# Performance work log

Measured on AMD Instinct MI355X. Metric: run time of the kernel, lower is better.

## Reference

```python
import jax, jax.numpy as jnp
import numpy as np

NUM_HEADS = 12
TOP_K = 2
ROPE_THETA = 10000.0
EPS = 1e-6

def _rmsnorm(x, w):
    return x * jax.lax.rsqrt(jnp.mean(x * x, axis=-1, keepdims=True) + EPS) * w

def _rotate_half(t):
    t1, t2 = jnp.split(t, 2, axis=-1)
    return jnp.concatenate([-t2, t1], axis=-1)

def setup_inputs() -> dict:
    key = jax.random.key(0)
    ks = jax.random.split(key, 8)
    B, S, H, E, F = 2, 2048, 768, 8, 3072
    s = 0.02
    return {
        "x": jax.random.normal(ks[0], (B, S, H), dtype=jnp.float32),
        "attn_norm_w": jnp.ones((H,), dtype=jnp.float32),
        "wqkv": jax.random.normal(ks[1], (H, 3 * H), dtype=jnp.float32) * s,
        "wo": jax.random.normal(ks[2], (H, H), dtype=jnp.float32) * s,
        "ffn_norm_w": jnp.ones((H,), dtype=jnp.float32),
        "router_w": jax.random.normal(ks[3], (H, E), dtype=jnp.float32) * s,
        "w1": jax.random.normal(ks[4], (E, H, F), dtype=jnp.float32) * s,
        "w2": jax.random.normal(ks[5], (E, F, H), dtype=jnp.float32) * s,
    }

def reference(x, attn_norm_w, wqkv, wo, ffn_norm_w, router_w, w1, w2):
    B, S, H = x.shape
    NH, Dh = NUM_HEADS, H // NUM_HEADS
    E = router_w.shape[1]

    # ---- attention sub-block: x = x + attn(rmsnorm(x)) ----
    h = _rmsnorm(x, attn_norm_w)
    qkv = h @ wqkv  # (B,S,3H)
    q, k, v = [t.reshape(B, S, NH, Dh) for t in jnp.split(qkv, 3, axis=-1)]

    # RoPE (llama-style half-split rotation)
    half = Dh // 2
    inv_freq = 1.0 / (ROPE_THETA ** (jnp.arange(half, dtype=jnp.float32) / half))
    ang = jnp.arange(S, dtype=jnp.float32)[:, None] * inv_freq[None, :]  # (S, half)
    cos = jnp.concatenate([jnp.cos(ang)] * 2, axis=-1)[None, :, None, :].astype(x.dtype)
    sin = jnp.concatenate([jnp.sin(ang)] * 2, axis=-1)[None, :, None, :].astype(x.dtype)
    q = q * cos + _rotate_half(q) * sin
    k = k * cos + _rotate_half(k) * sin

    scores = jnp.einsum('bqhd,bkhd->bhqk', q, k) / jnp.sqrt(jnp.asarray(Dh, x.dtype))
    causal = jnp.tril(jnp.ones((S, S), dtype=bool))
    scores = jnp.where(causal[None, None], scores, jnp.asarray(-1e9, x.dtype))
    attn = jax.nn.softmax(scores, axis=-1)
    o = jnp.einsum('bhqk,bkhd->bqhd', attn, v).reshape(B, S, H) @ wo
    x = x + o

    # ---- MoE FFN sub-block: x = x + moe(rmsnorm(x)) ----
    hn = _rmsnorm(x, ffn_norm_w).reshape(-1, H)  # (T,H)
    logits = hn @ router_w  # (T,E)
    probs = jax.nn.softmax(logits, axis=-1)
    top_v, top_i = jax.lax.top_k(probs, TOP_K)  # (T,K)
    top_v = top_v / jnp.sum(top_v, axis=-1, keepdims=True)
    onehot = jax.nn.one_hot(top_i, E, dtype=x.dtype)  # (T,K,E)
    combine = jnp.einsum('tke,tk->te', onehot, top_v)  # (T,E)

    h1 = jnp.einsum('th,ehf->etf', hn, w1)
    h2 = jnp.einsum('etf,efh->eth', jax.nn.silu(h1), w2)
    moe_out = jnp.einsum('eth,te->th', h2, combine).reshape(B, S, H)

    # load-balancing aux loss (switch-style)
    frac = jnp.mean(jnp.sum(onehot, axis=1), axis=0) / TOP_K  # (E,)
    mean_prob = jnp.mean(probs, axis=0)  # (E,)
    aux = jnp.asarray(E, x.dtype) * jnp.sum(frac * mean_prob)

    return (x + moe_out, aux)
```

## Files before the change

kernel.cpp:

```cpp
#include <hip/hip_runtime.h>
#include <cstdint>
#include <cstddef>

typedef __bf16 bf16;
typedef bf16 bf16x8 __attribute__((ext_vector_type(8)));
typedef float f32x4 __attribute__((ext_vector_type(4)));

__device__ __forceinline__ void async_cp16(const void* g, void* l) {
    __builtin_amdgcn_global_load_lds(
        (const __attribute__((address_space(1))) unsigned int*)(unsigned long long)g,
        (__attribute__((address_space(3))) unsigned int*)(unsigned int)(unsigned long long)l,
        16, 0, 0);
}

#define BARX() __builtin_amdgcn_s_barrier()
#define LGKM0() asm volatile("s_waitcnt lgkmcnt(0)" ::: "memory")
#define VMC4() asm volatile("s_waitcnt vmcnt(4)" ::: "memory")
#define VMC0() asm volatile("s_waitcnt vmcnt(0)" ::: "memory")

__global__ __launch_bounds__(256) void transpose_cast(const float* __restrict__ in,
                                                      bf16* __restrict__ out, int R, int C) {
    __shared__ float tile[32][33];
    int bz = blockIdx.z;
    in  += (size_t)bz * R * C;
    out += (size_t)bz * R * C;
    int c0 = blockIdx.x * 32, r0 = blockIdx.y * 32;
    int tx = threadIdx.x & 31, ty = threadIdx.x >> 5;
#pragma unroll
    for (int i = 0; i < 4; ++i)
        tile[ty + i * 8][tx] = in[(size_t)(r0 + ty + i * 8) * C + c0 + tx];
    __syncthreads();
#pragma unroll
    for (int i = 0; i < 4; ++i)
        out[(size_t)(c0 + ty + i * 8) * R + r0 + tx] = (bf16)tile[tx][ty + i * 8];
}

__global__ __launch_bounds__(256) void rmsnorm_cast(const float* __restrict__ x,
                                                    const float* __restrict__ w,
                                                    bf16* __restrict__ out) {
    int row = blockIdx.x, tid = threadIdx.x;
    const float* xr = x + (size_t)row * 768;
    float v0 = xr[tid], v1 = xr[tid + 256], v2 = xr[tid + 512];
    float s = v0 * v0 + v1 * v1 + v2 * v2;
#pragma unroll
    for (int off = 32; off; off >>= 1) s += __shfl_xor(s, off, 64);
    __shared__ float red[4];
    if ((tid & 63) == 0) red[tid >> 6] = s;
    __syncthreads();
    float tot = red[0] + red[1] + red[2] + red[3];
    float rs = rsqrtf(tot * (1.f / 768.f) + 1e-6f);
    bf16* o = out + (size_t)row * 768;
    o[tid]       = (bf16)(v0 * rs * w[tid]);
    o[tid + 256] = (bf16)(v1 * rs * w[tid + 256]);
    o[tid + 512] = (bf16)(v2 * rs * w[tid + 512]);
}

__global__ __launch_bounds__(256) void rope_kernel(const bf16* __restrict__ qkv,
                                                   bf16* __restrict__ qb,
                                                   bf16* __restrict__ kb,
                                                   bf16* __restrict__ vtb) {
    __shared__ float vs[64][65];
    const int tid = threadIdx.x;
    const int s0 = blockIdx.x * 64, bh = blockIdx.y;
    const int b = bh / 12, h = bh - b * 12;
    const float qscale = 0.18033688f;
#pragma unroll
    for (int i = 0; i < 16; ++i) {
        int idx = i * 256 + tid;
        int sl = idx >> 6, d = idx & 63;
        int sg = s0 + sl;
        size_t base = ((size_t)b * 2048 + sg) * 2304;
        float qv = (float)qkv[base + h * 64 + d];
        float kv = (float)qkv[base + 768 + h * 64 + d];
        float vv = (float)qkv[base + 1536 + h * 64 + d];
        float qp = (float)qkv[base + h * 64 + (d ^ 32)];
        float kp = (float)qkv[base + 768 + h * 64 + (d ^ 32)];
        int jj = d & 31;
        float invf = __expf(-(float)jj * (9.210340371976184f / 32.f));
        float ang = (float)sg * invf;
        float cv, sv;
        __sincosf(ang, &sv, &cv);
        float rq = (d < 32) ? -qp : qp;
        float rk = (d < 32) ? -kp : kp;
        qb[((size_t)bh * 2048 + sg) * 64 + d] = (bf16)((qv * cv + rq * sv) * qscale);
        kb[((size_t)bh * 2048 + sg) * 64 + d] = (bf16)(kv * cv + rk * sv);
        vs[sl][d] = vv;
    }
    __syncthreads();
#pragma unroll
    for (int i = 0; i < 16; ++i) {
        int idx = i * 256 + tid;
        int d = idx >> 6, sl = idx & 63;
        vtb[(size_t)bh * 64 * 2048 + (size_t)d * 2048 + s0 + sl] = (bf16)vs[sl][d];
    }
}

__global__ __launch_bounds__(256) void attn_kernel(const bf16* __restrict__ qb,
                                                   const bf16* __restrict__ kb,
                                                   const bf16* __restrict__ vtb,
                                                   bf16* __restrict__ ob) {
    __shared__ __align__(16) bf16 Qs[2][64][32];
    __shared__ __align__(16) bf16 Ks[2][2][64][32];
    __shared__ __align__(16) bf16 Vts[2][2][64][32];
    __shared__ __align__(16) bf16 Ps[4][1024];

    const int tid = threadIdx.x, lane = tid & 63, w = tid >> 6;
    const int quad = lane >> 4, l16 = lane & 15;
    const int linear = (int)blockIdx.y * 32 + (int)blockIdx.x;
    const int xcd = linear & 7, j = linear >> 3;
    const int bh = xcd * 3 + (j >> 5);
    const int qt = 31 - (j & 31);
    const int q0 = qt * 64;
    const int b = bh / 12, h = bh - b * 12;

    const bf16* qhead = qb + (size_t)bh * 2048 * 64;
    const bf16* khead = kb + (size_t)bh * 2048 * 64;
    const bf16* vthead = vtb + (size_t)bh * 64 * 2048;

#pragma unroll
    for (int i = 0; i < 2; ++i) {
        int o = (i * 256 + tid) * 16;
        int kk = o >> 12, row = (o >> 6) & 63, el = (o & 63) >> 1;
        async_cp16(qhead + (size_t)(q0 + row) * 64 + kk * 32 + el,
                   (char*)Qs + (size_t)(i * 256 + w * 64) * 16);
    }
    __syncthreads();
    bf16x8 bq[2];
#pragma unroll
    for (int kk = 0; kk < 2; ++kk)
        bq[kk] = *(const bf16x8*)&Qs[kk][w * 16 + l16][quad * 8];

    f32x4 o_acc[4] = {};
    float m_st = -1e30f, l_st = 0.f;

    for (int j2 = 0; j2 <= qt; j2 += 2) {
        int nt2 = (j2 + 1 <= qt) ? 2 : 1;
        __syncthreads();
#pragma unroll
        for (int t = 0; t < 2; ++t) {
            if (t >= nt2) break;
            int kv0 = (j2 + t) * 64;
#pragma unroll
            for (int i = 0; i < 2; ++i) {
                int o = (i * 256 + tid) * 16;
                int kk = o >> 12, row = (o >> 6) & 63, el = (o & 63) >> 1;
                async_cp16(khead + (size_t)(kv0 + row) * 64 + kk * 32 + el,
                           (char*)&Ks[t] + (size_t)(i * 256 + w * 64) * 16);
                async_cp16(vthead + (size_t)row * 2048 + kv0 + kk * 32 + el,
                           (char*)&Vts[t] + (size_t)(i * 256 + w * 64) * 16);
            }
        }
        __syncthreads();

#pragma unroll
        for (int t = 0; t < 2; ++t) {
            if (t >= nt2) break;

            f32x4 sacc[4] = {};
#pragma unroll
            for (int kk = 0; kk < 2; ++kk) {
                bf16x8 ak[4];
#pragma unroll
                for (int ni = 0; ni < 4; ++ni)
                    ak[ni] = *(const bf16x8*)&Ks[t][kk][ni * 16 + l16][quad * 8];
#pragma unroll
                for (int ni = 0; ni < 4; ++ni)
                    sacc[ni] = __builtin_amdgcn_mfma_f32_16x16x32_bf16(ak[ni], bq[kk], sacc[ni], 0, 0, 0);
            }

            if (j2 + t == qt) {
                int ql = w * 16 + l16;
#pragma unroll
                for (int ni = 0; ni < 4; ++ni)
#pragma unroll
                    for (int r = 0; r < 4; ++r)
                        if (ni * 16 + quad * 4 + r > ql) sacc[ni][r] = -1e30f;
            }

            float mx = sacc[0][0];
#pragma unroll
            for (int ni = 0; ni < 4; ++ni)
#pragma unroll
                for (int r = 0; r < 4; ++r) mx = fmaxf(mx, sacc[ni][r]);
            mx = fmaxf(mx, __shfl_xor(mx, 16, 64));
            mx = fmaxf(mx, __shfl_xor(mx, 32, 64));
            float mnew = fmaxf(m_st, mx);
            float alpha = exp2f(m_st - mnew);
            m_st = mnew;
            float rsum = 0.f;
#pragma unroll
            for (int ni = 0; ni < 4; ++ni)
#pragma unroll
                for (int r = 0; r < 4; ++r) {
                    float pv = exp2f(sacc[ni][r] - mnew);
                    sacc[ni][r] = pv;
                    rsum += pv;
                }
            rsum += __shfl_xor(rsum, 16, 64);
            rsum += __shfl_xor(rsum, 32, 64);
            l_st = l_st * alpha + rsum;

            float af[4];
#pragma unroll
            for (int r = 0; r < 4; ++r) af[r] = __shfl(alpha, quad * 4 + r, 64);
#pragma unroll
            for (int ni = 0; ni < 4; ++ni)
#pragma unroll
                for (int r = 0; r < 4; ++r) o_acc[ni][r] *= af[r];

            bf16* pb = Ps[w];
#pragma unroll
            for (int ni = 0; ni < 4; ++ni)
#pragma unroll
                for (int r = 0; r < 4; ++r) {
                    int kv = ni * 16 + quad * 4 + r;
                    int ch = (kv >> 3) ^ (l16 & 7);
                    pb[l16 * 64 + ch * 8 + (kv & 7)] = (bf16)sacc[ni][r];
                }

#pragma unroll
            for (int kk = 0; kk < 2; ++kk) {
                int ch = (kk * 4 + quad) ^ (l16 & 7);
                bf16x8 ap = *(const bf16x8*)&pb[l16 * 64 + ch * 8];
                bf16x8 bv[4];
#pragma unroll
                for (int ni = 0; ni < 4; ++ni)
                    bv[ni] = *(const bf16x8*)&Vts[t][kk][ni * 16 + l16][quad * 8];
#pragma unroll
                for (int ni = 0; ni < 4; ++ni)
                    o_acc[ni] = __builtin_amdgcn_mfma_f32_16x16x32_bf16(ap, bv[ni], o_acc[ni], 0, 0, 0);
            }
        }
    }

    float lf[4];
#pragma unroll
    for (int r = 0; r < 4; ++r) lf[r] = 1.f / __shfl(l_st, quad * 4 + r, 64);
#pragma unroll
    for (int ni = 0; ni < 4; ++ni)
#pragma unroll
        for (int r = 0; r < 4; ++r) {
            int rowg = q0 + w * 16 + quad * 4 + r;
            size_t tk = (size_t)b * 2048 + rowg;
            ob[tk * 768 + h * 64 + ni * 16 + l16] = (bf16)(o_acc[ni][r] * lf[r]);
        }
}

__global__ __launch_bounds__(256) void rms_router(const float* __restrict__ x1,
                                                  const float* __restrict__ w,
                                                  const float* __restrict__ rw,
                                                  bf16* __restrict__ hn,
                                                  int* __restrict__ topi,
                                                  float* __restrict__ topw,
                                                  float* __restrict__ probsb) {
    __shared__ float hnf[768];
    __shared__ float part[256];
    __shared__ float lg[8];
    __shared__ float probs[8];
    __shared__ float red[4];
    int row = blockIdx.x, tid = threadIdx.x;
    const float* xr = x1 + (size_t)row * 768;
    float v0 = xr[tid], v1 = xr[tid + 256], v2 = xr[tid + 512];
    float s = v0 * v0 + v1 * v1 + v2 * v2;
#pragma unroll
    for (int off = 32; off; off >>= 1) s += __shfl_xor(s, off, 64);
    if ((tid & 63) == 0) red[tid >> 6] = s;
    __syncthreads();
    float tot = red[0] + red[1] + red[2] + red[3];
    float rs = rsqrtf(tot * (1.f / 768.f) + 1e-6f);
    float h0 = v0 * rs * w[tid], h1v = v1 * rs * w[tid + 256], h2v = v2 * rs * w[tid + 512];
    hnf[tid] = h0; hnf[tid + 256] = h1v; hnf[tid + 512] = h2v;
    bf16* o = hn + (size_t)row * 768;
    o[tid] = (bf16)h0; o[tid + 256] = (bf16)h1v; o[tid + 512] = (bf16)h2v;
    __syncthreads();
    int e = tid & 7, seg = tid >> 3;
    float p = 0.f;
#pragma unroll
    for (int j = 0; j < 24; ++j) { int k = seg * 24 + j; p += hnf[k] * rw[k * 8 + e]; }
    part[tid] = p;
    __syncthreads();
    if (tid < 8) { float a = 0.f; for (int sgi = 0; sgi < 32; ++sgi) a += part[sgi * 8 + tid]; lg[tid] = a; }
    __syncthreads();
    if (tid == 0) {
        float mx = lg[0];
        for (int i = 1; i < 8; ++i) mx = fmaxf(mx, lg[i]);
        float ssum = 0.f, ex[8];
        for (int i = 0; i < 8; ++i) { ex[i] = __expf(lg[i] - mx); ssum += ex[i]; }
        float inv = 1.f / ssum;
        for (int i = 0; i < 8; ++i) probs[i] = ex[i] * inv;
        int e0 = 0; float p0 = probs[0];
        for (int i = 1; i < 8; ++i) if (probs[i] > p0) { p0 = probs[i]; e0 = i; }
        int e1 = -1; float p1 = -1.f;
        for (int i = 0; i < 8; ++i) if (i != e0 && probs[i] > p1) { p1 = probs[i]; e1 = i; }
        float wsum = p0 + p1;
        topi[row * 2] = e0; topi[row * 2 + 1] = e1;
        topw[row * 2] = p0 / wsum; topw[row * 2 + 1] = p1 / wsum;
    }
    __syncthreads();
    if (tid < 8) probsb[(size_t)row * 8 + tid] = probs[tid];
}

__global__ __launch_bounds__(256) void router_stats(const float* __restrict__ probsb,
                                                    const int* __restrict__ topi,
                                                    int* ctrl, int4* tiles, float* auxOut) {
    __shared__ float pws[4][8];
    __shared__ int cws[4][8];
    int tid = threadIdx.x;
    float s[8] = {};
    int cnt[8] = {};
    for (int t = tid; t < 4096; t += 256) {
        const float4* p = (const float4*)(probsb + (size_t)t * 8);
        float4 a = p[0], b = p[1];
        s[0] += a.x; s[1] += a.y; s[2] += a.z; s[3] += a.w;
        s[4] += b.x; s[5] += b.y; s[6] += b.z; s[7] += b.w;
        int e0 = topi[2 * t], e1 = topi[2 * t + 1];
#pragma unroll
        for (int e = 0; e < 8; ++e) cnt[e] += (e == e0) + (e == e1);
    }
#pragma unroll
    for (int e = 0; e < 8; ++e)
#pragma unroll
        for (int off = 32; off; off >>= 1) {
            s[e] += __shfl_xor(s[e], off, 64);
            cnt[e] += __shfl_xor(cnt[e], off, 64);
        }
    if ((tid & 63) == 0) {
#pragma unroll
        for (int e = 0; e < 8; ++e) { pws[tid >> 6][e] = s[e]; cws[tid >> 6][e] = cnt[e]; }
    }
    __syncthreads();
    if (tid == 0) {
        int off = 0, nt = 0;
        float aux = 0.f;
        for (int e = 0; e < 8; ++e) {
            int ne = cws[0][e] + cws[1][e] + cws[2][e] + cws[3][e];
            float ps = pws[0][e] + pws[1][e] + pws[2][e] + pws[3][e];
            ctrl[e] = ne;
            ctrl[32 + e] = off;
            int ntl = (ne + 255) >> 8;
            for (int i = 0; i < ntl; ++i) { tiles[nt] = make_int4(e, off + i * 256, off + ne, 0); ++nt; }
            off += ntl << 8;
            aux += ((float)ne * (1.f / 8192.f)) * (ps * (1.f / 4096.f));
        }
        ctrl[24] = nt;
        auxOut[0] = 8.f * aux;
    }
}

__global__ __launch_bounds__(256) void place_tokens(const int* __restrict__ topi,
                                                    int* ctrl, int* __restrict__ perm,
                                                    int* __restrict__ tokslot) {
    __shared__ int lcnt[8], lbase[8];
    int tid = threadIdx.x;
    int t = blockIdx.x * 256 + tid;
    if (tid < 8) lcnt[tid] = 0;
    __syncthreads();
    int e0 = topi[2 * t], e1 = topi[2 * t + 1];
    int p0 = atomicAdd(&lcnt[e0], 1);
    int p1 = atomicAdd(&lcnt[e1], 1);
    __syncthreads();
    if (tid < 8) lbase[tid] = atomicAdd(&ctrl[16 + tid], lcnt[tid]);
    __syncthreads();
    int g0 = ctrl[32 + e0] + lbase[e0] + p0;
    int g1 = ctrl[32 + e1] + lbase[e1] + p1;
    perm[g0] = t; perm[g1] = t;
    tokslot[2 * t] = g0; tokslot[2 * t + 1] = g1;
}

__global__ __launch_bounds__(256) void moe_combine(const bf16* __restrict__ h2,
                                                   const int* __restrict__ tokslot,
                                                   const float* __restrict__ topw,
                                                   float* __restrict__ out) {
    int t = blockIdx.x, tid = threadIdx.x;
    int s0 = tokslot[2 * t], s1 = tokslot[2 * t + 1];
    float w0 = topw[2 * t], w1 = topw[2 * t + 1];
    const bf16* r0 = h2 + (size_t)s0 * 768;
    const bf16* r1 = h2 + (size_t)s1 * 768;
    float* o = out + (size_t)t * 768;
#pragma unroll
    for (int i = 0; i < 3; ++i) {
        int c = i * 256 + tid;
        o[c] += w0 * (float)r0[c] + w1 * (float)r1[c];
    }
}

template <int MODE>
__global__ __launch_bounds__(512, 2) void gemm8p(const bf16* __restrict__ A,
                                                 const bf16* __restrict__ Bt,
                                                 int N, int K,
                                                 bf16* __restrict__ outB,
                                                 const int4* __restrict__ tiles,
                                                 const int* __restrict__ ctrl,
                                                 const int* __restrict__ perm) {
    __shared__ __align__(16) bf16 As[2][2][128 * 64];
    __shared__ __align__(16) bf16 Bs[2][2][128 * 64];
    __shared__ int sPerm[256];

    const int tid = threadIdx.x, lane = tid & 63, wid = tid >> 6;
    const int wr = wid >> 2, wc = wid & 3;
    const int quad = lane >> 4, l16 = lane & 15;

    const int NB = N >> 8;
    const int mt = (int)blockIdx.x / NB;
    const int n0 = ((int)blockIdx.x % NB) << 8;

    int m0 = 0, row0 = 0;
    if (MODE == 0) {
        m0 = mt << 8;
    } else {
        if (mt >= ctrl[24]) return;
        int4 td = tiles[mt];
        row0 = td.y;
        Bt += (size_t)td.x * (size_t)N * K;
        if (tid < 256) {
            int g = row0 + tid;
            sPerm[tid] = perm[(g < td.z) ? g : row0];
        }
        __syncthreads();
    }

    const int r0t = tid >> 3;
    const int s0t = tid & 7;
    const int cOff = ((s0t ^ (r0t & 7)) << 3);
    const bf16* pA[2][2];
    const bf16* pB[2][2];
#pragma unroll
    for (int h = 0; h < 2; ++h)
#pragma unroll
        for (int i = 0; i < 2; ++i) {
            int rrow = h * 128 + i * 64 + r0t;
            pB[h][i] = Bt + (size_t)(n0 + rrow) * K + cOff;
            if (MODE == 0) pA[h][i] = A + (size_t)(m0 + rrow) * K + cOff;
            else           pA[h][i] = A + (size_t)sPerm[rrow] * K + cOff;
        }

    auto stA = [&](int buf, int h, int kt) {
#pragma unroll
        for (int i = 0; i < 2; ++i)
            async_cp16(pA[h][i] + kt, (char*)As[buf][h] + (size_t)((i * 512 + wid * 64) * 16));
    };
    auto stB = [&](int buf, int h, int kt) {
#pragma unroll
        for (int i = 0; i < 2; ++i)
            async_cp16(pB[h][i] + kt, (char*)Bs[buf][h] + (size_t)((i * 512 + wid * 64) * 16));
    };
    auto ldA = [&](int buf, int mi, int kk) -> bf16x8 {
        int r = mi * 16 + l16;
        int s = (kk * 4 + quad) ^ (l16 & 7);
        return *(const bf16x8*)((const char*)As[buf][wr] + r * 128 + s * 16);
    };
    auto ldB = [&](int buf, int ni, int kk) -> bf16x8 {
        int c = wc * 64 + ni * 16 + l16;
        int s = (kk * 4 + quad) ^ (l16 & 7);
        return *(const bf16x8*)((const char*)Bs[buf][c >> 7] + (c & 127) * 128 + s * 16);
    };

    f32x4 acc[8][4] = {};
    bf16x8 aLo[4][2], aHi[4][2], bLo[2][2], bHi[2][2];

    auto ktile = [&](int b, auto S1, auto S2, auto S3, auto S4, int vm) {
#pragma unroll
        for (int mi = 0; mi < 4; ++mi) { aLo[mi][0] = ldA(b, mi, 0); aLo[mi][1] = ldA(b, mi, 1); }
#pragma unroll
        for (int ni = 0; ni < 2; ++ni) { bLo[ni][0] = ldB(b, ni, 0); bLo[ni][1] = ldB(b, ni, 1); }
        S1();
        BARX(); LGKM0();
        __builtin_amdgcn_s_setprio(1);
#pragma unroll
        for (int mi = 0; mi < 4; ++mi)
#pragma unroll
            for (int ni = 0; ni < 2; ++ni) {
                acc[mi][ni] = __builtin_amdgcn_mfma_f32_16x16x32_bf16(aLo[mi][0], bLo[ni][0], acc[mi][ni], 0, 0, 0);
                acc[mi][ni] = __builtin_amdgcn_mfma_f32_16x16x32_bf16(aLo[mi][1], bLo[ni][1], acc[mi][ni], 0, 0, 0);
            }
        __builtin_amdgcn_s_setprio(0);
        BARX();
#pragma unroll
        for (int ni = 0; ni < 2; ++ni) { bHi[ni][0] = ldB(b, ni + 2, 0); bHi[ni][1] = ldB(b, ni + 2, 1); }
        S2();
        BARX(); LGKM0();
        __builtin_amdgcn_s_setprio(1);
#pragma unroll
        for (int mi = 0; mi < 4; ++mi)
#pragma unroll
            for (int ni = 0; ni < 2; ++ni) {
                acc[mi][ni + 2] = __builtin_amdgcn_mfma_f32_16x16x32_bf16(aLo[mi][0], bHi[ni][0], acc[mi][ni + 2], 0, 0, 0);
                acc[mi][ni + 2] = __builtin_amdgcn_mfma_f32_16x16x32_bf16(aLo[mi][1], bHi[ni][1], acc[mi][ni + 2], 0, 0, 0);
            }
        __builtin_amdgcn_s_setprio(0);
        BARX();
#pragma unroll
        for (int mi = 0; mi < 4; ++mi) { aHi[mi][0] = ldA(b, mi + 4, 0); aHi[mi][1] = ldA(b, mi + 4, 1); }
        S3();
        BARX(); LGKM0();
        __builtin_amdgcn_s_setprio(1);
#pragma unroll
        for (int mi = 0; mi < 4; ++mi)
#pragma unroll
            for (int ni = 0; ni < 2; ++ni) {
                acc[mi + 4][ni + 2] = __builtin_amdgcn_mfma_f32_16x16x32_bf16(aHi[mi][0], bHi[ni][0], acc[mi + 4][ni + 2], 0, 0, 0);
                acc[mi + 4][ni + 2] = __builtin_amdgcn_mfma_f32_16x16x32_bf16(aHi[mi][1], bHi[ni][1], acc[mi + 4][ni + 2], 0, 0, 0);
            }
        __builtin_amdgcn_s_setprio(0);
        BARX();
        S4();
        BARX(); LGKM0();
        __builtin_amdgcn_s_setprio(1);
#pragma unroll
        for (int mi = 0; mi < 4; ++mi)
#pragma unroll
            for (int ni = 0; ni < 2; ++ni) {
                acc[mi + 4][ni] = __builtin_amdgcn_mfma_f32_16x16x32_bf16(aHi[mi][0], bLo[ni][0], acc[mi + 4][ni], 0, 0, 0);
                acc[mi + 4][ni] = __builtin_amdgcn_mfma_f32_16x16x32_bf16(aHi[mi][1], bLo[ni][1], acc[mi + 4][ni], 0, 0, 0);
            }
        __builtin_amdgcn_s_setprio(0);
        if (vm == 4) { VMC4(); } else if (vm == 0) { VMC0(); }
        BARX();
    };

    stA(0, 0, 0); stA(0, 1, 0); stB(0, 0, 0); stB(0, 1, 0);
    stB(1, 0, 64); stB(1, 1, 64);
    VMC4();
    BARX();

    const int nIt = K >> 7;
    for (int it = 0; it < nIt; ++it) {
        const bool last = (it == nIt - 1);
        const int kA = (it * 2 + 1) << 6;
        const int kB = (it * 2 + 2) << 6;
        const int kC = (it * 2 + 3) << 6;
        ktile(0,
              [&] { stA(1, 0, kA); },
              [&] { stA(1, 1, kA); },
              [&] { if (!last) stB(0, 0, kB); },
              [&] { if (!last) stB(0, 1, kB); },
              last ? 0 : 4);
        ktile(1,
              [&] { if (!last) stA(0, 0, kB); },
              [&] { if (!last) stA(0, 1, kB); },
              [&] { if (!last) stB(1, 0, kC); },
              [&] { if (!last) stB(1, 1, kC); },
              last ? -1 : 4);
    }

#pragma unroll
    for (int mi = 0; mi < 8; ++mi)
#pragma unroll
        for (int ni = 0; ni < 4; ++ni)
#pragma unroll
            for (int r = 0; r < 4; ++r) {
                int lrow = wr * 128 + mi * 16 + quad * 4 + r;
                int col  = n0 + wc * 64 + ni * 16 + l16;
                float v = acc[mi][ni][r];
                if (MODE == 0) {
                    outB[(size_t)(m0 + lrow) * N + col] = (bf16)v;
                } else {
                    float sv = v / (1.f + __expf(-v));
                    outB[(size_t)(row0 + lrow) * N + col] = (bf16)sv;
                }
            }
}

template <int MODE, int NBX, int MTX>
__global__ __launch_bounds__(256) void gemm_nt(const bf16* __restrict__ A,
                                               const bf16* __restrict__ Bt,
                                               int N, int K,
                                               const float* __restrict__ xres,
                                               float* __restrict__ outF,
                                               bf16* __restrict__ outB,
                                               const int4* __restrict__ tiles,
                                               const int* __restrict__ ctrl,
                                               const int* __restrict__ perm) {
    __shared__ __align__(16) bf16 As[2][128 * 32];
    __shared__ __align__(16) bf16 Bs[2][128 * 32];
    __shared__ int sPerm[128];

    const int tid = threadIdx.x, lane = tid & 63, w = tid >> 6;
    const int wr = w >> 1, wc = w & 1, quad = lane >> 4, l16 = lane & 15;

    const int L = blockIdx.x;
    const int xcd = L & 7, j = L >> 3;
    const int mt = xcd * MTX + j / NBX;
    const int n0 = (j % NBX) * 128;

    int m0 = 0, row0 = 0;
    if (MODE <= 1) {
        m0 = mt * 128;
    } else if (MODE == 2) {
        if (mt >= ctrl[24]) return;
        int4 td = tiles[mt];
        row0 = td.y;
        int rowend = td.z;
        Bt += (size_t)td.x * N * K;
        if (tid < 128) {
            int g = row0 + tid;
            int gs = (g < rowend) ? g : row0;
            sPerm[tid] = perm[gs];
        }
        __syncthreads();
    } else {
        int tt = mt >> 1;
        if (tt >= ctrl[24]) return;
        int4 td = tiles[tt];
        row0 = td.y + ((mt & 1) << 7);
        Bt += (size_t)td.x * N * K;
    }

    auto stage = [&](int buf, int kt) {
#pragma unroll
        for (int i = 0; i < 2; ++i) {
            int c = i * 256 + tid;
            int r = c >> 2, koff = (c & 3) * 8;
            const bf16* gp;
            if (MODE == 2)      gp = A + (size_t)sPerm[r] * K + kt + koff;
            else if (MODE == 3) gp = A + (size_t)(row0 + r) * K + kt + koff;
            else                gp = A + (size_t)(m0 + r) * K + kt + koff;
            async_cp16(gp, (char*)As[buf] + (size_t)(i * 256 + w * 64) * 16);
            async_cp16(Bt + (size_t)(n0 + r) * K + kt + koff,
                       (char*)Bs[buf] + (size_t)(i * 256 + w * 64) * 16);
        }
    };

    f32x4 acc[4][4] = {};
    const int nIt = K >> 5;
    stage(0, 0);

    for (int it = 0; it < nIt; ++it) {
        const int cur = it & 1;
        __syncthreads();
        if (it + 1 < nIt) stage(cur ^ 1, (it + 1) << 5);

        bf16x8 af[4], bfr[4];
#pragma unroll
        for (int mi = 0; mi < 4; ++mi)
            af[mi] = *(const bf16x8*)(As[cur] + (wr * 64 + mi * 16 + l16) * 32 + quad * 8);
#pragma unroll
        for (int ni = 0; ni < 4; ++ni)
            bfr[ni] = *(const bf16x8*)(Bs[cur] + (wc * 64 + ni * 16 + l16) * 32 + quad * 8);
#pragma unroll
        for (int mi = 0; mi < 4; ++mi)
#pragma unroll
            for (int ni = 0; ni < 4; ++ni)
                acc[mi][ni] = __builtin_amdgcn_mfma_f32_16x16x32_bf16(af[mi], bfr[ni], acc[mi][ni], 0, 0, 0);
    }

#pragma unroll
    for (int mi = 0; mi < 4; ++mi)
#pragma unroll
        for (int ni = 0; ni < 4; ++ni)
#pragma unroll
            for (int r = 0; r < 4; ++r) {
                int lrow = wr * 64 + mi * 16 + quad * 4 + r;
                int col = n0 + wc * 64 + ni * 16 + l16;
                float v = acc[mi][ni][r];
                if (MODE == 0) {
                    outB[(size_t)(m0 + lrow) * N + col] = (bf16)v;
                } else if (MODE == 1) {
                    size_t idx = (size_t)(m0 + lrow) * N + col;
                    outF[idx] = v + xres[idx];
                } else if (MODE == 2) {
                    float sv = v / (1.f + __expf(-v));
                    outB[(size_t)(row0 + lrow) * N + col] = (bf16)sv;
                } else {
                    outB[(size_t)(row0 + lrow) * N + col] = (bf16)v;
                }
            }
}

__global__ void zero_ctrl(int* ctrl) { if (threadIdx.x < 64) ctrl[threadIdx.x] = 0; }

extern "C" void kernel_launch(void* const* d_in, const int* in_sizes, int n_in,
                              void* d_out, int out_size, void* d_ws, size_t ws_size,
                              hipStream_t stream) {
    const float* x    = (const float*)d_in[0];
    const float* anw  = (const float*)d_in[1];
    const float* wqkv = (const float*)d_in[2];
    const float* wo   = (const float*)d_in[3];
    const float* fnw  = (const float*)d_in[4];
    const float* rw   = (const float*)d_in[5];
    const float* w1   = (const float*)d_in[6];
    const float* w2   = (const float*)d_in[7];
    float* out = (float*)d_out;

    char* ws = (char*)d_ws;
    size_t off = 0;
    auto alloc = [&](size_t bytes) -> char* {
        char* p = ws + off;
        off = (off + bytes + 255) & ~(size_t)255;
        return p;
    };
    bf16* wqkvT = (bf16*)alloc(2304ull * 768 * 2);
    bf16* woT   = (bf16*)alloc(768ull * 768 * 2);
    bf16* w1T   = (bf16*)alloc(8ull * 3072 * 768 * 2);
    bf16* w2T   = (bf16*)alloc(8ull * 768 * 3072 * 2);
    bf16* hbuf  = (bf16*)alloc(4096ull * 768 * 2);
    bf16* qkvb  = (bf16*)alloc(4096ull * 2304 * 2);
    bf16* qb    = (bf16*)alloc(24ull * 2048 * 64 * 2);
    bf16* kb    = (bf16*)alloc(24ull * 2048 * 64 * 2);
    bf16* vtb   = (bf16*)alloc(24ull * 64 * 2048 * 2);
    bf16* obuf  = (bf16*)alloc(4096ull * 768 * 2);
    bf16* hn    = (bf16*)alloc(4096ull * 768 * 2);
    int*  topi  = (int*)alloc(4096ull * 2 * 4);
    float* topw = (float*)alloc(4096ull * 2 * 4);
    float* probsb = (float*)alloc(4096ull * 8 * 4);
    int*  ctrl  = (int*)alloc(64 * 4);
    int4* tiles = (int4*)alloc(80 * 16);
    int*  perm  = (int*)alloc(10240 * 4);
    int*  tokslot = (int*)alloc(4096ull * 2 * 4);
    bf16* h1    = (bf16*)alloc(10240ull * 3072 * 2);
    bf16* h2    = qkvb;
    (void)ws_size; (void)in_sizes; (void)n_in;

    zero_ctrl<<<1, 64, 0, stream>>>(ctrl);
    transpose_cast<<<dim3(72, 24, 1), 256, 0, stream>>>(wqkv, wqkvT, 768, 2304);
    transpose_cast<<<dim3(24, 24, 1), 256, 0, stream>>>(wo, woT, 768, 768);
    transpose_cast<<<dim3(96, 24, 8), 256, 0, stream>>>(w1, w1T, 768, 3072);
    transpose_cast<<<dim3(24, 96, 8), 256, 0, stream>>>(w2, w2T, 3072, 768);
    rmsnorm_cast<<<4096, 256, 0, stream>>>(x, anw, hbuf);
    gemm8p<0><<<144, 512, 0, stream>>>(hbuf, wqkvT, 2304, 768, qkvb, nullptr, nullptr, nullptr);
    rope_kernel<<<dim3(32, 24), 256, 0, stream>>>(qkvb, qb, kb, vtb);
    attn_kernel<<<dim3(32, 24), 256, 0, stream>>>(qb, kb, vtb, obuf);
    gemm_nt<1, 6, 4><<<192, 256, 0, stream>>>(obuf, woT, 768, 768,
                                              x, out, nullptr, nullptr, nullptr, nullptr);
    rms_router<<<4096, 256, 0, stream>>>(out, fnw, rw, hn, topi, topw, probsb);
    router_stats<<<1, 256, 0, stream>>>(probsb, topi, ctrl, tiles, out + (out_size - 1));
    place_tokens<<<16, 256, 0, stream>>>(topi, ctrl, perm, tokslot);
    gemm8p<2><<<480, 512, 0, stream>>>(hn, w1T, 3072, 768, h1, tiles, ctrl, perm);
    gemm_nt<3, 6, 10><<<480, 256, 0, stream>>>(h1, w2T, 768, 3072,
                                               nullptr, nullptr, h2, tiles, ctrl, perm);
    moe_combine<<<4096, 256, 0, stream>>>(h2, tokslot, topw, out);
}
```

Measured before the change: 500.4 us.

## Run MoE down-projection on 256x256 gemm8p with split-K and fp32 partials

The second expert GEMM moves from the 128x128 gemm_nt kernel to the larger 256x256 gemm8p kernel, with K split in two. The two halves write fp32 partial sums into a scratch area that reuses the w1T buffer, and moe_combine adds the partials during the weighted combine. gemm8p's pipeline is also simplified to a single k-tile loop that prefetches two tiles ahead, and a launch-order remap spreads blocks across the XCDs. This trades heavier combine traffic (four fp32 row reads per token instead of two bf16) for better MFMA reuse and more workgroups in the large GEMM.

```diff
diff --git a/kernel.cpp b/kernel.cpp
--- a/kernel.cpp
+++ b/kernel.cpp
@@ -5,6 +5,8 @@
 typedef __bf16 bf16;
 typedef bf16 bf16x8 __attribute__((ext_vector_type(8)));
 typedef float f32x4 __attribute__((ext_vector_type(4)));
+
+static constexpr size_t SKS = (size_t)10240 * 768;
 
 __device__ __forceinline__ void async_cp16(const void* g, void* l) {
     __builtin_amdgcn_global_load_lds(
@@ -15,7 +17,7 @@
 
 #define BARX() __builtin_amdgcn_s_barrier()
 #define LGKM0() asm volatile("s_waitcnt lgkmcnt(0)" ::: "memory")
-#define VMC4() asm volatile("s_waitcnt vmcnt(4)" ::: "memory")
+#define VMC8() asm volatile("s_waitcnt vmcnt(8)" ::: "memory")
 #define VMC0() asm volatile("s_waitcnt vmcnt(0)" ::: "memory")
 
 __global__ __launch_bounds__(256) void transpose_cast(const float* __restrict__ in,
@@ -367,31 +369,36 @@
     tokslot[2 * t] = g0; tokslot[2 * t + 1] = g1;
 }
 
-__global__ __launch_bounds__(256) void moe_combine(const bf16* __restrict__ h2,
+__global__ __launch_bounds__(256) void moe_combine(const float* __restrict__ h2p,
                                                    const int* __restrict__ tokslot,
                                                    const float* __restrict__ topw,
                                                    float* __restrict__ out) {
     int t = blockIdx.x, tid = threadIdx.x;
     int s0 = tokslot[2 * t], s1 = tokslot[2 * t + 1];
     float w0 = topw[2 * t], w1 = topw[2 * t + 1];
-    const bf16* r0 = h2 + (size_t)s0 * 768;
-    const bf16* r1 = h2 + (size_t)s1 * 768;
+    const float* a0 = h2p + (size_t)s0 * 768;
+    const float* a1 = h2p + SKS + (size_t)s0 * 768;
+    const float* b0 = h2p + (size_t)s1 * 768;
+    const float* b1 = h2p + SKS + (size_t)s1 * 768;
     float* o = out + (size_t)t * 768;
 #pragma unroll
     for (int i = 0; i < 3; ++i) {
         int c = i * 256 + tid;
-        o[c] += w0 * (float)r0[c] + w1 * (float)r1[c];
-    }
-}
-
-template <int MODE>
+        o[c] += w0 * (a0[c] + a1[c]) + w1 * (b0[c] + b1[c]);
+    }
+}
+
+template <int MODE, int KTOT, int SK>
 __global__ __launch_bounds__(512, 2) void gemm8p(const bf16* __restrict__ A,
                                                  const bf16* __restrict__ Bt,
-                                                 int N, int K,
+                                                 int N,
                                                  bf16* __restrict__ outB,
+                                                 float* __restrict__ outF,
                                                  const int4* __restrict__ tiles,
                                                  const int* __restrict__ ctrl,
                                                  const int* __restrict__ perm) {
+    constexpr int KB = KTOT / SK;
+    constexpr int nT = KB >> 6;
     __shared__ __align__(16) bf16 As[2][2][128 * 64];
     __shared__ __align__(16) bf16 Bs[2][2][128 * 64];
     __shared__ int sPerm[256];
@@ -401,8 +408,14 @@
     const int quad = lane >> 4, l16 = lane & 15;
 
     const int NB = N >> 8;
-    const int mt = (int)blockIdx.x / NB;
-    const int n0 = ((int)blockIdx.x % NB) << 8;
+    const int nwg = (int)gridDim.x, q8 = nwg >> 3;
+    const int L = (int)blockIdx.x;
+    const int lin = (L & 7) * q8 + (L >> 3);
+    int mt, nb, sk = 0;
+    if (SK == 2) { int d = NB * 2; mt = lin / d; int r = lin - mt * d; nb = r >> 1; sk = r & 1; }
+    else         { mt = lin / NB; nb = lin - mt * NB; }
+    const int n0 = nb << 8;
+    const int k0 = sk * KB;
 
     int m0 = 0, row0 = 0;
     if (MODE == 0) {
@@ -411,38 +424,46 @@
         if (mt >= ctrl[24]) return;
         int4 td = tiles[mt];
         row0 = td.y;
-        Bt += (size_t)td.x * (size_t)N * K;
-        if (tid < 256) {
-            int g = row0 + tid;
-            sPerm[tid] = perm[(g < td.z) ? g : row0];
+        Bt += (size_t)td.x * (size_t)N * KTOT;
+        if (MODE == 2) {
+            if (tid < 256) {
+                int g = row0 + tid;
+                sPerm[tid] = perm[(g < td.z) ? g : row0];
+            }
+            __syncthreads();
         }
-        __syncthreads();
-    }
-
-    const int r0t = tid >> 3;
-    const int s0t = tid & 7;
+    }
+
+    const int r0t = tid >> 3, s0t = tid & 7;
     const int cOff = ((s0t ^ (r0t & 7)) << 3);
-    const bf16* pA[2][2];
-    const bf16* pB[2][2];
+    unsigned aOff[2][2], bOff[2][2];
 #pragma unroll
     for (int h = 0; h < 2; ++h)
 #pragma unroll
         for (int i = 0; i < 2; ++i) {
             int rrow = h * 128 + i * 64 + r0t;
-            pB[h][i] = Bt + (size_t)(n0 + rrow) * K + cOff;
-            if (MODE == 0) pA[h][i] = A + (size_t)(m0 + rrow) * K + cOff;
-            else           pA[h][i] = A + (size_t)sPerm[rrow] * K + cOff;
+            bOff[h][i] = (unsigned)((((n0 + rrow) * KTOT) + k0 + cOff) * 2);
+            int ar = (MODE == 0) ? (m0 + rrow) : (MODE == 2 ? sPerm[rrow] : row0 + rrow);
+            aOff[h][i] = (unsigned)(((ar * KTOT) + k0 + cOff) * 2);
         }
-
-    auto stA = [&](int buf, int h, int kt) {
-#pragma unroll
-        for (int i = 0; i < 2; ++i)
-            async_cp16(pA[h][i] + kt, (char*)As[buf][h] + (size_t)((i * 512 + wid * 64) * 16));
+    const char* Ab = (const char*)A;
+    const char* Bb = (const char*)Bt;
+
+    auto stA = [&](int buf, int ktB) {
+#pragma unroll
+        for (int h = 0; h < 2; ++h)
+#pragma unroll
+            for (int i = 0; i < 2; ++i)
+                async_cp16(Ab + aOff[h][i] + ktB,
+                           (char*)As[buf][h] + (size_t)((i * 512 + wid * 64) * 16));
     };
-    auto stB = [&](int buf, int h, int kt) {
-#pragma unroll
-        for (int i = 0; i < 2; ++i)
-            async_cp16(pB[h][i] + kt, (char*)Bs[buf][h] + (size_t)((i * 512 + wid * 64) * 16));
+    auto stB = [&](int buf, int ktB) {
+#pragma unroll
+        for (int h = 0; h < 2; ++h)
+#pragma unroll
+            for (int i = 0; i < 2; ++i)
+                async_cp16(Bb + bOff[h][i] + ktB,
+                           (char*)Bs[buf][h] + (size_t)((i * 512 + wid * 64) * 16));
     };
     auto ldA = [&](int buf, int mi, int kk) -> bf16x8 {
         int r = mi * 16 + l16;
@@ -458,12 +479,19 @@
     f32x4 acc[8][4] = {};
     bf16x8 aLo[4][2], aHi[4][2], bLo[2][2], bHi[2][2];
 
-    auto ktile = [&](int b, auto S1, auto S2, auto S3, auto S4, int vm) {
+    stA(0, 0); stB(0, 0); stA(1, 128); stB(1, 128);
+    VMC8();
+    BARX();
+
+    for (int t = 0; t < nT; ++t) {
+        const int b = t & 1;
+        const bool st = (t + 2 < nT);
+        const int ktB = (t + 2) << 7;
+
 #pragma unroll
         for (int mi = 0; mi < 4; ++mi) { aLo[mi][0] = ldA(b, mi, 0); aLo[mi][1] = ldA(b, mi, 1); }
 #pragma unroll
         for (int ni = 0; ni < 2; ++ni) { bLo[ni][0] = ldB(b, ni, 0); bLo[ni][1] = ldB(b, ni, 1); }
-        S1();
         BARX(); LGKM0();
         __builtin_amdgcn_s_setprio(1);
 #pragma unroll
@@ -475,9 +503,9 @@
             }
         __builtin_amdgcn_s_setprio(0);
         BARX();
+
 #pragma unroll
         for (int ni = 0; ni < 2; ++ni) { bHi[ni][0] = ldB(b, ni + 2, 0); bHi[ni][1] = ldB(b, ni + 2, 1); }
-        S2();
         BARX(); LGKM0();
         __builtin_amdgcn_s_setprio(1);
 #pragma unroll
@@ -489,9 +517,10 @@
             }
         __builtin_amdgcn_s_setprio(0);
         BARX();
+
 #pragma unroll
         for (int mi = 0; mi < 4; ++mi) { aHi[mi][0] = ldA(b, mi + 4, 0); aHi[mi][1] = ldA(b, mi + 4, 1); }
-        S3();
+        if (st) stB(b, ktB);
         BARX(); LGKM0();
         __builtin_amdgcn_s_setprio(1);
 #pragma unroll
@@ -503,8 +532,9 @@
             }
         __builtin_amdgcn_s_setprio(0);
         BARX();
-        S4();
-        BARX(); LGKM0();
+
+        if (st) stA(b, ktB);
+        BARX();
         __builtin_amdgcn_s_setprio(1);
 #pragma unroll
         for (int mi = 0; mi < 4; ++mi)
@@ -514,33 +544,8 @@
                 acc[mi + 4][ni] = __builtin_amdgcn_mfma_f32_16x16x32_bf16(aHi[mi][1], bLo[ni][1], acc[mi + 4][ni], 0, 0, 0);
             }
         __builtin_amdgcn_s_setprio(0);
-        if (vm == 4) { VMC4(); } else if (vm == 0) { VMC0(); }
+        if (st) { VMC8(); } else if (t + 2 == nT) { VMC0(); }
         BARX();
-    };
-
-    stA(0, 0, 0); stA(0, 1, 0); stB(0, 0, 0); stB(0, 1, 0);
-    stB(1, 0, 64); stB(1, 1, 64);
-    VMC4();
-    BARX();
-
-    const int nIt = K >> 7;
-    for (int it = 0; it < nIt; ++it) {
-        const bool last = (it == nIt - 1);
-        const int kA = (it * 2 + 1) << 6;
-        const int kB = (it * 2 + 2) << 6;
-        const int kC = (it * 2 + 3) << 6;
-        ktile(0,
-              [&] { stA(1, 0, kA); },
-              [&] { stA(1, 1, kA); },
-              [&] { if (!last) stB(0, 0, kB); },
-              [&] { if (!last) stB(0, 1, kB); },
-              last ? 0 : 4);
-        ktile(1,
-              [&] { if (!last) stA(0, 0, kB); },
-              [&] { if (!last) stA(0, 1, kB); },
-              [&] { if (!last) stB(1, 0, kC); },
-              [&] { if (!last) stB(1, 1, kC); },
-              last ? -1 : 4);
     }
 
 #pragma unroll
@@ -554,9 +559,11 @@
                 float v = acc[mi][ni][r];
                 if (MODE == 0) {
                     outB[(size_t)(m0 + lrow) * N + col] = (bf16)v;
-                } else {
+                } else if (MODE == 2) {
                     float sv = v / (1.f + __expf(-v));
                     outB[(size_t)(row0 + lrow) * N + col] = (bf16)sv;
+                } else {
+                    outF[(size_t)sk * SKS + (size_t)(row0 + lrow) * N + col] = v;
                 }
             }
 }
@@ -567,13 +574,9 @@
                                                int N, int K,
                                                const float* __restrict__ xres,
                                                float* __restrict__ outF,
-                                               bf16* __restrict__ outB,
-                                               const int4* __restrict__ tiles,
-                                               const int* __restrict__ ctrl,
-                                               const int* __restrict__ perm) {
+                                               bf16* __restrict__ outB) {
     __shared__ __align__(16) bf16 As[2][128 * 32];
     __shared__ __align__(16) bf16 Bs[2][128 * 32];
-    __shared__ int sPerm[128];
 
     const int tid = threadIdx.x, lane = tid & 63, w = tid >> 6;
     const int wr = w >> 1, wc = w & 1, quad = lane >> 4, l16 = lane & 15;
@@ -582,40 +585,15 @@
     const int xcd = L & 7, j = L >> 3;
     const int mt = xcd * MTX + j / NBX;
     const int n0 = (j % NBX) * 128;
-
-    int m0 = 0, row0 = 0;
-    if (MODE <= 1) {
-        m0 = mt * 128;
-    } else if (MODE == 2) {
-        if (mt >= ctrl[24]) return;
-        int4 td = tiles[mt];
-        row0 = td.y;
-        int rowend = td.z;
-        Bt += (size_t)td.x * N * K;
-        if (tid < 128) {
-            int g = row0 + tid;
-            int gs = (g < rowend) ? g : row0;
-            sPerm[tid] = perm[gs];
-        }
-        __syncthreads();
-    } else {
-        int tt = mt >> 1;
-        if (tt >= ctrl[24]) return;
-        int4 td = tiles[tt];
-        row0 = td.y + ((mt & 1) << 7);
-        Bt += (size_t)td.x * N * K;
-    }
+    const int m0 = mt * 128;
 
     auto stage = [&](int buf, int kt) {
 #pragma unroll
         for (int i = 0; i < 2; ++i) {
             int c = i * 256 + tid;
             int r = c >> 2, koff = (c & 3) * 8;
-            const bf16* gp;
-            if (MODE == 2)      gp = A + (size_t)sPerm[r] * K + kt + koff;
-            else if (MODE == 3) gp = A + (size_t)(row0 + r) * K + kt + koff;
-            else                gp = A + (size_t)(m0 + r) * K + kt + koff;
-            async_cp16(gp, (char*)As[buf] + (size_t)(i * 256 + w * 64) * 16);
+            async_cp16(A + (size_t)(m0 + r) * K + kt + koff,
+                       (char*)As[buf] + (size_t)(i * 256 + w * 64) * 16);
             async_cp16(Bt + (size_t)(n0 + r) * K + kt + koff,
                        (char*)Bs[buf] + (size_t)(i * 256 + w * 64) * 16);
         }
@@ -653,16 +631,11 @@
                 int lrow = wr * 64 + mi * 16 + quad * 4 + r;
                 int col = n0 + wc * 64 + ni * 16 + l16;
                 float v = acc[mi][ni][r];
-                if (MODE == 0) {
-                    outB[(size_t)(m0 + lrow) * N + col] = (bf16)v;
-                } else if (MODE == 1) {
+                if (MODE == 1) {
                     size_t idx = (size_t)(m0 + lrow) * N + col;
                     outF[idx] = v + xres[idx];
-                } else if (MODE == 2) {
-                    float sv = v / (1.f + __expf(-v));
-                    outB[(size_t)(row0 + lrow) * N + col] = (bf16)sv;
                 } else {
-                    outB[(size_t)(row0 + lrow) * N + col] = (bf16)v;
+                    outB[(size_t)(m0 + lrow) * N + col] = (bf16)v;
                 }
             }
 }
@@ -691,8 +664,8 @@
     };
     bf16* wqkvT = (bf16*)alloc(2304ull * 768 * 2);
     bf16* woT   = (bf16*)alloc(768ull * 768 * 2);
+    bf16* w2T   = (bf16*)alloc(8ull * 768 * 3072 * 2);
     bf16* w1T   = (bf16*)alloc(8ull * 3072 * 768 * 2);
-    bf16* w2T   = (bf16*)alloc(8ull * 768 * 3072 * 2);
     bf16* hbuf  = (bf16*)alloc(4096ull * 768 * 2);
     bf16* qkvb  = (bf16*)alloc(4096ull * 2304 * 2);
     bf16* qb    = (bf16*)alloc(24ull * 2048 * 64 * 2);
@@ -708,7 +681,7 @@
     int*  perm  = (int*)alloc(10240 * 4);
     int*  tokslot = (int*)alloc(4096ull * 2 * 4);
     bf16* h1    = (bf16*)alloc(10240ull * 3072 * 2);
-    bf16* h2    = qkvb;
+    float* h2p  = (float*)w1T;
     (void)ws_size; (void)in_sizes; (void)n_in;
 
     zero_ctrl<<<1, 64, 0, stream>>>(ctrl);
@@ -717,16 +690,17 @@
     transpose_cast<<<dim3(96, 24, 8), 256, 0, stream>>>(w1, w1T, 768, 3072);
     transpose_cast<<<dim3(24, 96, 8), 256, 0, stream>>>(w2, w2T, 3072, 768);
     rmsnorm_cast<<<4096, 256, 0, stream>>>(x, anw, hbuf);
-    gemm8p<0><<<144, 512, 0, stream>>>(hbuf, wqkvT, 2304, 768, qkvb, nullptr, nullptr, nullptr);
+    gemm8p<0, 768, 1><<<144, 512, 0, stream>>>(hbuf, wqkvT, 2304, qkvb, nullptr,
+                                               nullptr, nullptr, nullptr);
     rope_kernel<<<dim3(32, 24), 256, 0, stream>>>(qkvb, qb, kb, vtb);
     attn_kernel<<<dim3(32, 24), 256, 0, stream>>>(qb, kb, vtb, obuf);
-    gemm_nt<1, 6, 4><<<192, 256, 0, stream>>>(obuf, woT, 768, 768,
-                                              x, out, nullptr, nullptr, nullptr, nullptr);
+    gemm_nt<1, 6, 4><<<192, 256, 0, stream>>>(obuf, woT, 768, 768, x, out, nullptr);
     rms_router<<<4096, 256, 0, stream>>>(out, fnw, rw, hn, topi, topw, probsb);
     router_stats<<<1, 256, 0, stream>>>(probsb, topi, ctrl, tiles, out + (out_size - 1));
     place_tokens<<<16, 256, 0, stream>>>(topi, ctrl, perm, tokslot);
-    gemm8p<2><<<480, 512, 0, stream>>>(hn, w1T, 3072, 768, h1, tiles, ctrl, perm);
-    gemm_nt<3, 6, 10><<<480, 256, 0, stream>>>(h1, w2T, 768, 3072,
-                                               nullptr, nullptr, h2, tiles, ctrl, perm);
-    moe_combine<<<4096, 256, 0, stream>>>(h2, tokslot, topw, out);
-}
+    gemm8p<2, 768, 1><<<480, 512, 0, stream>>>(hn, w1T, 3072, h1, nullptr,
+                                               tiles, ctrl, perm);
+    gemm8p<3, 3072, 2><<<240, 512, 0, stream>>>(h1, w2T, 768, nullptr, h2p,
+                                                tiles, ctrl, perm);
+    moe_combine<<<4096, 256, 0, stream>>>(h2p, tokslot, topw, out);
+}
```

After: 502.3 us. About the same (+0.4%).
